# Kernel optimization log

Measured on AMD Instinct MI355X. Metric: run time of the kernel, lower is better.

Reference implementation:

```python
import jax, jax.numpy as jnp
import numpy as np

HEAD_SIZE = 64
EMBED_DIM = 1024

def setup_inputs() -> dict:
    key = jax.random.key(0)
    kx, kq, kk, kv = jax.random.split(key, 4)
    B, T, C, H = 8, 2048, EMBED_DIM, HEAD_SIZE
    scale = 1.0 / np.sqrt(C)
    x = jax.random.normal(kx, (B, T, C), dtype=jnp.float32)
    # nn.Linear(C, H, bias=False): weight (H, C); store as (C, H) for x @ W
    Wq = jax.random.normal(kq, (C, H), dtype=jnp.float32) * scale
    Wk = jax.random.normal(kk, (C, H), dtype=jnp.float32) * scale
    Wv = jax.random.normal(kv, (C, H), dtype=jnp.float32) * scale
    return {"x": x, "Wq": Wq, "Wk": Wk, "Wv": Wv}

def reference(x, Wq, Wk, Wv):
    B, T, C = x.shape
    H = Wq.shape[1]
    q = x @ Wq  # (B, T, H)
    k = x @ Wk
    v = x @ Wv
    # scaled scores with causal mask (tril)
    wei = jnp.einsum('bth,bsh->bts', q, k) * (H ** -0.5)  # (B, T, T)
    causal = jnp.tril(jnp.ones((T, T), dtype=bool))
    wei = jnp.where(causal, wei, -jnp.inf)
    wei = jax.nn.softmax(wei, axis=-1)
    out = jnp.einsum('bts,bsh->bth', wei, v)  # (B, T, H)
    return out
```

## Files before the change

### kernel.cpp

```cpp
#include <hip/hip_runtime.h>

#define T_SEQ 2048
#define C_DIM 1024
#define H_DIM 64
#define B_DIM 8
#define NROW (B_DIM * T_SEQ)

typedef __attribute__((ext_vector_type(8))) short short8;
typedef __attribute__((ext_vector_type(4))) float f32x4;

__device__ __forceinline__ short f2bf(float f) {
  unsigned u = __builtin_bit_cast(unsigned, f);
  u += 0x7fffu + ((u >> 16) & 1u);
  return (short)(u >> 16);
}

__global__ __launch_bounds__(256) void w_prep(
    const float* __restrict__ Wq, const float* __restrict__ Wk,
    const float* __restrict__ Wv, short* __restrict__ Wt2) {
  const int unit = blockIdx.x * 256 + threadIdx.x;
  const int lane = unit & 63;
  const int t = unit >> 6;
  const int kh = t & 3;
  const int g = t >> 2;
  const int ntg = g % 12;
  const int kc = g / 12;
  const int n16 = lane & 15, quad = lane >> 4;
  const int mat = ntg >> 2;
  const int h = (ntg & 3) * 16 + n16;
  const int kb = kc * 128 + kh * 32 + quad * 8;
  const float* W = (mat == 0) ? Wq : (mat == 1 ? Wk : Wv);
  short8 v;
#pragma unroll
  for (int e = 0; e < 8; ++e) v[e] = f2bf(W[(size_t)(kb + e) * H_DIM + h]);
  *(short8*)(Wt2 + (size_t)unit * 8) = v;
}

__device__ __forceinline__ int lds_addr(int tile, int kh, int qd, int nn) {
  return tile * 2048 + kh * 512 + (qd * 16 + (nn ^ ((kh * 4 + qd) & 7))) * 8;
}

__global__ __launch_bounds__(256, 2) void qkv_gemm(
    const float* __restrict__ x, const short* __restrict__ Wt2,
    short* __restrict__ q, short* __restrict__ k, short* __restrict__ vt) {
  __shared__ __align__(16) short As[2][4096];
  const int tid = threadIdx.x;
  const int w = tid >> 6, lane = tid & 63;
  const int n16 = lane & 15, quad = lane >> 4;
  const int row0 = blockIdx.x * 32;

  f32x4 acc[2][3];
#pragma unroll
  for (int mt = 0; mt < 2; ++mt)
#pragma unroll
    for (int ln = 0; ln < 3; ++ln) acc[mt][ln] = (f32x4){0.f, 0.f, 0.f, 0.f};

  const int u20 = tid, u21 = 256 + tid;
  const int sr0 = u20 >> 4, f0 = u20 & 15;
  const int sr1 = u21 >> 4, f1 = u21 & 15;
  const float* ap0 = x + (size_t)(row0 + sr0) * C_DIM + f0 * 8;
  const float* ap1 = x + (size_t)(row0 + sr1) * C_DIM + f1 * 8;
  const int soff0 = lds_addr(sr0 >> 4, f0 >> 2, f0 & 3, sr0 & 15);
  const int soff1 = lds_addr(sr1 >> 4, f1 >> 2, f1 & 3, sr1 & 15);

  int swz[4];
#pragma unroll
  for (int kh = 0; kh < 4; ++kh)
    swz[kh] = (quad * 16 + (n16 ^ ((kh * 4 + quad) & 7))) * 8;

  const short* bbase = Wt2 + (size_t)(w * 3) * 2048 + (size_t)lane * 8;

  float4 astg[2][4];
  short8 bfr[12];

#define STAGE_A(d, p)                                      \
  {                                                        \
    short8 av0, av1;                                       \
    _Pragma("unroll") for (int e = 0; e < 4; ++e) {        \
      av0[e] = f2bf(((const float*)&astg[d][0])[e]);       \
      av0[e + 4] = f2bf(((const float*)&astg[d][1])[e]);   \
      av1[e] = f2bf(((const float*)&astg[d][2])[e]);       \
      av1[e + 4] = f2bf(((const float*)&astg[d][3])[e]);   \
    }                                                      \
    *(short8*)(&As[p][0] + soff0) = av0;                   \
    *(short8*)(&As[p][0] + soff1) = av1;                   \
  }

  astg[0][0] = *(const float4*)(ap0);
  astg[0][1] = *(const float4*)(ap0 + 4);
  astg[0][2] = *(const float4*)(ap1);
  astg[0][3] = *(const float4*)(ap1 + 4);
  astg[1][0] = *(const float4*)(ap0 + 128);
  astg[1][1] = *(const float4*)(ap0 + 132);
  astg[1][2] = *(const float4*)(ap1 + 128);
  astg[1][3] = *(const float4*)(ap1 + 132);
#pragma unroll
  for (int ln = 0; ln < 3; ++ln)
#pragma unroll
    for (int kh = 0; kh < 4; ++kh)
      bfr[ln * 4 + kh] = *(const short8*)(bbase + ln * 2048 + kh * 512);
  STAGE_A(0, 0);
  asm volatile("s_waitcnt lgkmcnt(0)" ::: "memory");
  __builtin_amdgcn_sched_barrier(0);
  __builtin_amdgcn_s_barrier();
  __builtin_amdgcn_sched_barrier(0);

#pragma unroll
  for (int kc = 0; kc < 8; ++kc) {
    const short* asb = &As[kc & 1][0];
#pragma unroll
    for (int kh = 0; kh < 4; ++kh) {
      const short8 a0 = *(const short8*)(asb + kh * 512 + swz[kh]);
      const short8 a1 = *(const short8*)(asb + 2048 + kh * 512 + swz[kh]);
#pragma unroll
      for (int ln = 0; ln < 3; ++ln) {
        acc[0][ln] = __builtin_amdgcn_mfma_f32_16x16x32_bf16(
            a0, bfr[ln * 4 + kh], acc[0][ln], 0, 0, 0);
        acc[1][ln] = __builtin_amdgcn_mfma_f32_16x16x32_bf16(
            a1, bfr[ln * 4 + kh], acc[1][ln], 0, 0, 0);
      }
    }
    if (kc < 7) {
      const short* bc = bbase + (size_t)(kc + 1) * 24576;
#pragma unroll
      for (int ln = 0; ln < 3; ++ln)
#pragma unroll
        for (int kh = 0; kh < 4; ++kh)
          bfr[ln * 4 + kh] = *(const short8*)(bc + ln * 2048 + kh * 512);
      if (kc < 6) {
        astg[kc & 1][0] = *(const float4*)(ap0 + (kc + 2) * 128);
        astg[kc & 1][1] = *(const float4*)(ap0 + (kc + 2) * 128 + 4);
        astg[kc & 1][2] = *(const float4*)(ap1 + (kc + 2) * 128);
        astg[kc & 1][3] = *(const float4*)(ap1 + (kc + 2) * 128 + 4);
      }
      STAGE_A((kc + 1) & 1, (kc + 1) & 1);
      asm volatile("s_waitcnt lgkmcnt(0)" ::: "memory");
      __builtin_amdgcn_sched_barrier(0);
      __builtin_amdgcn_s_barrier();
      __builtin_amdgcn_sched_barrier(0);
    }
  }
#undef STAGE_A

  const int b = row0 >> 11;
#pragma unroll
  for (int mt = 0; mt < 2; ++mt)
#pragma unroll
    for (int ln = 0; ln < 3; ++ln) {
      const int ntg = w * 3 + ln;
      const int mat = ntg >> 2;
      const int cl = (ntg & 3) * 16 + n16;
#pragma unroll
      for (int r = 0; r < 4; ++r) {
        const int row = row0 + mt * 16 + quad * 4 + r;
        const float v = acc[mt][ln][r];
        if (mat == 0)
          q[(size_t)row * H_DIM + cl] = f2bf(v * 0.125f);
        else if (mat == 1)
          k[(size_t)row * H_DIM + cl] = f2bf(v);
        else
          vt[((size_t)b * H_DIM + cl) * T_SEQ + (row & (T_SEQ - 1))] = f2bf(v);
      }
    }
}

__global__ __launch_bounds__(256) void attn_mfma(
    const short* __restrict__ q, const short* __restrict__ k,
    const short* __restrict__ vt, float* __restrict__ out) {
  __shared__ __align__(16) short pbuf[4][1024];
  __shared__ __align__(16) float oshare[3][1024];
  __shared__ __align__(16) float lshare[3][256];
  const int tid = threadIdx.x;
  const int w = tid >> 6;
  const int lane = tid & 63;
  const int n16 = lane & 15, quad = lane >> 4;
  const int b = blockIdx.x & 7;
  const int qt = (T_SEQ / 16 - 1) - (blockIdx.x >> 3);
  const int r0 = qt * 16;

  const short* qb = q + ((size_t)b * T_SEQ + r0) * H_DIM;
  const short* kb = k + (size_t)b * T_SEQ * H_DIM;
  const short* vb = vt + (size_t)b * H_DIM * T_SEQ;

  const short8 aq0 = *(const short8*)(qb + (size_t)n16 * H_DIM + quad * 8);
  const short8 aq1 = *(const short8*)(qb + (size_t)n16 * H_DIM + 32 + quad * 8);

  f32x4 O[4];
#pragma unroll
  for (int i = 0; i < 4; ++i) O[i] = (f32x4){0.f, 0.f, 0.f, 0.f};
  float lsum[4] = {0.f, 0.f, 0.f, 0.f};

  const int nj = (r0 + 16 + 63) >> 6;
  for (int jt = w; jt < nj; jt += 4) {
    const int j0 = jt * 64;

    short8 bk[4][2];
#pragma unroll
    for (int nt = 0; nt < 4; ++nt) {
      const short* kp = kb + (size_t)(j0 + nt * 16 + n16) * H_DIM + quad * 8;
      bk[nt][0] = *(const short8*)kp;
      bk[nt][1] = *(const short8*)(kp + 32);
    }

    f32x4 s[4];
#pragma unroll
    for (int nt = 0; nt < 4; ++nt) {
      f32x4 z = (f32x4){0.f, 0.f, 0.f, 0.f};
      z = __builtin_amdgcn_mfma_f32_16x16x32_bf16(aq0, bk[nt][0], z, 0, 0, 0);
      z = __builtin_amdgcn_mfma_f32_16x16x32_bf16(aq1, bk[nt][1], z, 0, 0, 0);
      s[nt] = z;
    }

    const bool full = (j0 + 64 <= r0);
#pragma unroll
    for (int nt = 0; nt < 4; ++nt) {
      const int base =
          (nt >> 1) * 512 + ((((nt & 1) << 1) | (n16 >> 3)) * 128) + (n16 & 7);
#pragma unroll
      for (int r = 0; r < 4; ++r) {
        float p;
        if (full) {
          p = __expf(s[nt][r]);
        } else {
          const int j = j0 + nt * 16 + n16;
          const int row = r0 + quad * 4 + r;
          p = (j <= row) ? __expf(s[nt][r]) : 0.f;
        }
        lsum[r] += p;
        pbuf[w][base + (quad * 4 + r) * 8] = f2bf(p);
      }
    }

    short8 bv[4][2];
#pragma unroll
    for (int ht = 0; ht < 4; ++ht)
#pragma unroll
      for (int kh = 0; kh < 2; ++kh)
        bv[ht][kh] = *(const short8*)(vb + (size_t)(ht * 16 + n16) * T_SEQ +
                                      j0 + kh * 32 + quad * 8);

    const short8 ap0 = *(const short8*)(&pbuf[w][0] + lane * 8);
    const short8 ap1 = *(const short8*)(&pbuf[w][0] + 512 + lane * 8);

#pragma unroll
    for (int ht = 0; ht < 4; ++ht) {
      O[ht] = __builtin_amdgcn_mfma_f32_16x16x32_bf16(ap0, bv[ht][0], O[ht], 0, 0, 0);
      O[ht] = __builtin_amdgcn_mfma_f32_16x16x32_bf16(ap1, bv[ht][1], O[ht], 0, 0, 0);
    }
  }

  if (w != 0) {
#pragma unroll
    for (int ht = 0; ht < 4; ++ht)
#pragma unroll
      for (int r = 0; r < 4; ++r)
        oshare[w - 1][(ht * 4 + r) * 64 + lane] = O[ht][r];
#pragma unroll
    for (int r = 0; r < 4; ++r) lshare[w - 1][r * 64 + lane] = lsum[r];
  }
  __syncthreads();
  if (w == 0) {
#pragma unroll
    for (int ht = 0; ht < 4; ++ht)
#pragma unroll
      for (int r = 0; r < 4; ++r) {
        float a = O[ht][r];
#pragma unroll
        for (int ow = 0; ow < 3; ++ow) a += oshare[ow][(ht * 4 + r) * 64 + lane];
        O[ht][r] = a;
      }
#pragma unroll
    for (int r = 0; r < 4; ++r) {
      float vsum = lsum[r];
#pragma unroll
      for (int ow = 0; ow < 3; ++ow) vsum += lshare[ow][r * 64 + lane];
      vsum += __shfl_xor(vsum, 1);
      vsum += __shfl_xor(vsum, 2);
      vsum += __shfl_xor(vsum, 4);
      vsum += __shfl_xor(vsum, 8);
      lsum[r] = vsum;
    }
#pragma unroll
    for (int ht = 0; ht < 4; ++ht)
#pragma unroll
      for (int r = 0; r < 4; ++r)
        out[((size_t)b * T_SEQ + r0 + quad * 4 + r) * H_DIM + ht * 16 + n16] =
            O[ht][r] / lsum[r];
  }
}

extern "C" void kernel_launch(void* const* d_in, const int* in_sizes, int n_in,
                              void* d_out, int out_size, void* d_ws,
                              size_t ws_size, hipStream_t stream) {
  const float* x = (const float*)d_in[0];
  const float* Wq = (const float*)d_in[1];
  const float* Wk = (const float*)d_in[2];
  const float* Wv = (const float*)d_in[3];

  char* ws = (char*)d_ws;
  short* Wt = (short*)ws;
  short* q = (short*)(ws + 3 * 64 * 1024 * 2);
  short* kk = (short*)(ws + 3 * 64 * 1024 * 2 + 2097152);
  short* vt = (short*)(ws + 3 * 64 * 1024 * 2 + 2 * 2097152);

  w_prep<<<96, 256, 0, stream>>>(Wq, Wk, Wv, Wt);
  qkv_gemm<<<NROW / 32, 256, 0, stream>>>(x, Wt, q, kk, vt);
  attn_mfma<<<B_DIM * (T_SEQ / 16), 256, 0, stream>>>(q, kk, vt, (float*)d_out);
}
```

Measured before the change: 143.2 us.

## Pair short and long causal query tiles per block to share K/V loads

Each attention block now handles two 16-row query tiles, one near the start and one near the end of the sequence (pa and 127-pa). This balances causal work across blocks and reuses each loaded K and V tile for both query tiles where they overlap. It halves the grid and doubles LDS use and per-thread accumulators, which raises register pressure and may lower occupancy.

```diff
diff --git a/kernel.cpp b/kernel.cpp
--- a/kernel.cpp
+++ b/kernel.cpp
@@ -167,32 +167,44 @@
 __global__ __launch_bounds__(256) void attn_mfma(
     const short* __restrict__ q, const short* __restrict__ k,
     const short* __restrict__ vt, float* __restrict__ out) {
-  __shared__ __align__(16) short pbuf[4][1024];
-  __shared__ __align__(16) float oshare[3][1024];
-  __shared__ __align__(16) float lshare[3][256];
+  __shared__ __align__(16) short pbuf[4][2048];
+  __shared__ __align__(16) float oshare[3][2048];
+  __shared__ __align__(16) float lshare[3][512];
   const int tid = threadIdx.x;
   const int w = tid >> 6;
   const int lane = tid & 63;
   const int n16 = lane & 15, quad = lane >> 4;
   const int b = blockIdx.x & 7;
-  const int qt = (T_SEQ / 16 - 1) - (blockIdx.x >> 3);
-  const int r0 = qt * 16;
-
-  const short* qb = q + ((size_t)b * T_SEQ + r0) * H_DIM;
+  const int pa = blockIdx.x >> 3;
+  const int r0a = pa * 16;
+  const int r0b = (127 - pa) * 16;
+
   const short* kb = k + (size_t)b * T_SEQ * H_DIM;
   const short* vb = vt + (size_t)b * H_DIM * T_SEQ;
-
-  const short8 aq0 = *(const short8*)(qb + (size_t)n16 * H_DIM + quad * 8);
-  const short8 aq1 = *(const short8*)(qb + (size_t)n16 * H_DIM + 32 + quad * 8);
-
-  f32x4 O[4];
-#pragma unroll
-  for (int i = 0; i < 4; ++i) O[i] = (f32x4){0.f, 0.f, 0.f, 0.f};
-  float lsum[4] = {0.f, 0.f, 0.f, 0.f};
-
-  const int nj = (r0 + 16 + 63) >> 6;
+  const short* qpa = q + ((size_t)b * T_SEQ + r0a) * H_DIM;
+  const short* qpb = q + ((size_t)b * T_SEQ + r0b) * H_DIM;
+
+  short8 aqA[2], aqB[2];
+  aqA[0] = *(const short8*)(qpa + (size_t)n16 * H_DIM + quad * 8);
+  aqA[1] = *(const short8*)(qpa + (size_t)n16 * H_DIM + 32 + quad * 8);
+  aqB[0] = *(const short8*)(qpb + (size_t)n16 * H_DIM + quad * 8);
+  aqB[1] = *(const short8*)(qpb + (size_t)n16 * H_DIM + 32 + quad * 8);
+
+  f32x4 OA[4], OB[4];
+#pragma unroll
+  for (int i = 0; i < 4; ++i) {
+    OA[i] = (f32x4){0.f, 0.f, 0.f, 0.f};
+    OB[i] = (f32x4){0.f, 0.f, 0.f, 0.f};
+  }
+  float lsA[4] = {0.f, 0.f, 0.f, 0.f};
+  float lsB[4] = {0.f, 0.f, 0.f, 0.f};
+
+  const int nj = (r0b + 16 + 63) >> 6;
+  const int njA = (r0a + 16 + 63) >> 6;
+
   for (int jt = w; jt < nj; jt += 4) {
     const int j0 = jt * 64;
+    const bool actA = (jt < njA);
 
     short8 bk[4][2];
 #pragma unroll
@@ -202,16 +214,26 @@
       bk[nt][1] = *(const short8*)(kp + 32);
     }
 
-    f32x4 s[4];
+    f32x4 sB[4];
 #pragma unroll
     for (int nt = 0; nt < 4; ++nt) {
       f32x4 z = (f32x4){0.f, 0.f, 0.f, 0.f};
-      z = __builtin_amdgcn_mfma_f32_16x16x32_bf16(aq0, bk[nt][0], z, 0, 0, 0);
-      z = __builtin_amdgcn_mfma_f32_16x16x32_bf16(aq1, bk[nt][1], z, 0, 0, 0);
-      s[nt] = z;
-    }
-
-    const bool full = (j0 + 64 <= r0);
+      z = __builtin_amdgcn_mfma_f32_16x16x32_bf16(aqB[0], bk[nt][0], z, 0, 0, 0);
+      z = __builtin_amdgcn_mfma_f32_16x16x32_bf16(aqB[1], bk[nt][1], z, 0, 0, 0);
+      sB[nt] = z;
+    }
+    f32x4 sA[4];
+    if (actA) {
+#pragma unroll
+      for (int nt = 0; nt < 4; ++nt) {
+        f32x4 z = (f32x4){0.f, 0.f, 0.f, 0.f};
+        z = __builtin_amdgcn_mfma_f32_16x16x32_bf16(aqA[0], bk[nt][0], z, 0, 0, 0);
+        z = __builtin_amdgcn_mfma_f32_16x16x32_bf16(aqA[1], bk[nt][1], z, 0, 0, 0);
+        sA[nt] = z;
+      }
+    }
+
+    const bool fullB = (j0 + 64 <= r0b);
 #pragma unroll
     for (int nt = 0; nt < 4; ++nt) {
       const int base =
@@ -219,15 +241,36 @@
 #pragma unroll
       for (int r = 0; r < 4; ++r) {
         float p;
-        if (full) {
-          p = __expf(s[nt][r]);
+        if (fullB) {
+          p = __expf(sB[nt][r]);
         } else {
           const int j = j0 + nt * 16 + n16;
-          const int row = r0 + quad * 4 + r;
-          p = (j <= row) ? __expf(s[nt][r]) : 0.f;
+          const int row = r0b + quad * 4 + r;
+          p = (j <= row) ? __expf(sB[nt][r]) : 0.f;
         }
-        lsum[r] += p;
-        pbuf[w][base + (quad * 4 + r) * 8] = f2bf(p);
+        lsB[r] += p;
+        pbuf[w][1024 + base + (quad * 4 + r) * 8] = f2bf(p);
+      }
+    }
+    if (actA) {
+      const bool fullA = (j0 + 64 <= r0a);
+#pragma unroll
+      for (int nt = 0; nt < 4; ++nt) {
+        const int base =
+            (nt >> 1) * 512 + ((((nt & 1) << 1) | (n16 >> 3)) * 128) + (n16 & 7);
+#pragma unroll
+        for (int r = 0; r < 4; ++r) {
+          float p;
+          if (fullA) {
+            p = __expf(sA[nt][r]);
+          } else {
+            const int j = j0 + nt * 16 + n16;
+            const int row = r0a + quad * 4 + r;
+            p = (j <= row) ? __expf(sA[nt][r]) : 0.f;
+          }
+          lsA[r] += p;
+          pbuf[w][base + (quad * 4 + r) * 8] = f2bf(p);
+        }
       }
     }
 
@@ -239,13 +282,21 @@
         bv[ht][kh] = *(const short8*)(vb + (size_t)(ht * 16 + n16) * T_SEQ +
                                       j0 + kh * 32 + quad * 8);
 
-    const short8 ap0 = *(const short8*)(&pbuf[w][0] + lane * 8);
-    const short8 ap1 = *(const short8*)(&pbuf[w][0] + 512 + lane * 8);
-
+    const short8 apB0 = *(const short8*)(&pbuf[w][1024] + lane * 8);
+    const short8 apB1 = *(const short8*)(&pbuf[w][1536] + lane * 8);
 #pragma unroll
     for (int ht = 0; ht < 4; ++ht) {
-      O[ht] = __builtin_amdgcn_mfma_f32_16x16x32_bf16(ap0, bv[ht][0], O[ht], 0, 0, 0);
-      O[ht] = __builtin_amdgcn_mfma_f32_16x16x32_bf16(ap1, bv[ht][1], O[ht], 0, 0, 0);
+      OB[ht] = __builtin_amdgcn_mfma_f32_16x16x32_bf16(apB0, bv[ht][0], OB[ht], 0, 0, 0);
+      OB[ht] = __builtin_amdgcn_mfma_f32_16x16x32_bf16(apB1, bv[ht][1], OB[ht], 0, 0, 0);
+    }
+    if (actA) {
+      const short8 apA0 = *(const short8*)(&pbuf[w][0] + lane * 8);
+      const short8 apA1 = *(const short8*)(&pbuf[w][512] + lane * 8);
+#pragma unroll
+      for (int ht = 0; ht < 4; ++ht) {
+        OA[ht] = __builtin_amdgcn_mfma_f32_16x16x32_bf16(apA0, bv[ht][0], OA[ht], 0, 0, 0);
+        OA[ht] = __builtin_amdgcn_mfma_f32_16x16x32_bf16(apA1, bv[ht][1], OA[ht], 0, 0, 0);
+      }
     }
   }
 
@@ -253,10 +304,15 @@
 #pragma unroll
     for (int ht = 0; ht < 4; ++ht)
 #pragma unroll
-      for (int r = 0; r < 4; ++r)
-        oshare[w - 1][(ht * 4 + r) * 64 + lane] = O[ht][r];
-#pragma unroll
-    for (int r = 0; r < 4; ++r) lshare[w - 1][r * 64 + lane] = lsum[r];
+      for (int r = 0; r < 4; ++r) {
+        oshare[w - 1][(ht * 4 + r) * 64 + lane] = OA[ht][r];
+        oshare[w - 1][1024 + (ht * 4 + r) * 64 + lane] = OB[ht][r];
+      }
+#pragma unroll
+    for (int r = 0; r < 4; ++r) {
+      lshare[w - 1][r * 64 + lane] = lsA[r];
+      lshare[w - 1][256 + r * 64 + lane] = lsB[r];
+    }
   }
   __syncthreads();
   if (w == 0) {
@@ -264,28 +320,43 @@
     for (int ht = 0; ht < 4; ++ht)
 #pragma unroll
       for (int r = 0; r < 4; ++r) {
-        float a = O[ht][r];
-#pragma unroll
-        for (int ow = 0; ow < 3; ++ow) a += oshare[ow][(ht * 4 + r) * 64 + lane];
-        O[ht][r] = a;
+        float a = OA[ht][r], bb = OB[ht][r];
+#pragma unroll
+        for (int ow = 0; ow < 3; ++ow) {
+          a += oshare[ow][(ht * 4 + r) * 64 + lane];
+          bb += oshare[ow][1024 + (ht * 4 + r) * 64 + lane];
+        }
+        OA[ht][r] = a;
+        OB[ht][r] = bb;
       }
 #pragma unroll
     for (int r = 0; r < 4; ++r) {
-      float vsum = lsum[r];
-#pragma unroll
-      for (int ow = 0; ow < 3; ++ow) vsum += lshare[ow][r * 64 + lane];
-      vsum += __shfl_xor(vsum, 1);
-      vsum += __shfl_xor(vsum, 2);
-      vsum += __shfl_xor(vsum, 4);
-      vsum += __shfl_xor(vsum, 8);
-      lsum[r] = vsum;
+      float va = lsA[r], vb2 = lsB[r];
+#pragma unroll
+      for (int ow = 0; ow < 3; ++ow) {
+        va += lshare[ow][r * 64 + lane];
+        vb2 += lshare[ow][256 + r * 64 + lane];
+      }
+      va += __shfl_xor(va, 1);
+      va += __shfl_xor(va, 2);
+      va += __shfl_xor(va, 4);
+      va += __shfl_xor(va, 8);
+      vb2 += __shfl_xor(vb2, 1);
+      vb2 += __shfl_xor(vb2, 2);
+      vb2 += __shfl_xor(vb2, 4);
+      vb2 += __shfl_xor(vb2, 8);
+      lsA[r] = va;
+      lsB[r] = vb2;
     }
 #pragma unroll
     for (int ht = 0; ht < 4; ++ht)
 #pragma unroll
-      for (int r = 0; r < 4; ++r)
-        out[((size_t)b * T_SEQ + r0 + quad * 4 + r) * H_DIM + ht * 16 + n16] =
-            O[ht][r] / lsum[r];
+      for (int r = 0; r < 4; ++r) {
+        out[((size_t)b * T_SEQ + r0a + quad * 4 + r) * H_DIM + ht * 16 + n16] =
+            OA[ht][r] / lsA[r];
+        out[((size_t)b * T_SEQ + r0b + quad * 4 + r) * H_DIM + ht * 16 + n16] =
+            OB[ht][r] / lsB[r];
+      }
   }
 }
 
@@ -305,5 +376,5 @@
 
   w_prep<<<96, 256, 0, stream>>>(Wq, Wk, Wv, Wt);
   qkv_gemm<<<NROW / 32, 256, 0, stream>>>(x, Wt, q, kk, vt);
-  attn_mfma<<<B_DIM * (T_SEQ / 16), 256, 0, stream>>>(q, kk, vt, (float*)d_out);
-}
+  attn_mfma<<<B_DIM * (T_SEQ / 32), 256, 0, stream>>>(q, kk, vt, (float*)d_out);
+}
```

Result: faster. 137.0 us (-4.3%).

## Process four balanced query tiles per block and exchange P via lane shuffles

Applied to the files above, without the earlier changes.

Each attention block now handles four 16-row query tiles, paired front and back so causal work is balanced, and reuses each loaded K/V tile across all four. The QK^T MFMA is transposed so the P fragments can be rearranged into A-operand layout with cross-lane shuffles and packed bf16 conversion, replacing the LDS round-trip. Block count drops by four, which cuts redundant K/V loads. In exchange it raises register pressure (16 accumulators per wave) and LDS for the final reduction.

```diff
diff --git a/kernel.cpp b/kernel.cpp
--- a/kernel.cpp
+++ b/kernel.cpp
@@ -8,11 +8,18 @@
 
 typedef __attribute__((ext_vector_type(8))) short short8;
 typedef __attribute__((ext_vector_type(4))) float f32x4;
+typedef __attribute__((ext_vector_type(4))) int i32x4;
 
 __device__ __forceinline__ short f2bf(float f) {
   unsigned u = __builtin_bit_cast(unsigned, f);
   u += 0x7fffu + ((u >> 16) & 1u);
   return (short)(u >> 16);
+}
+
+__device__ __forceinline__ unsigned pk_bf16(float lo, float hi) {
+  unsigned r;
+  asm("v_cvt_pk_bf16_f32 %0, %1, %2" : "=v"(r) : "v"(lo), "v"(hi));
+  return r;
 }
 
 __global__ __launch_bounds__(256) void w_prep(
@@ -167,31 +174,42 @@
 __global__ __launch_bounds__(256) void attn_mfma(
     const short* __restrict__ q, const short* __restrict__ k,
     const short* __restrict__ vt, float* __restrict__ out) {
-  __shared__ __align__(16) short pbuf[4][1024];
-  __shared__ __align__(16) float oshare[3][1024];
-  __shared__ __align__(16) float lshare[3][256];
+  __shared__ __align__(16) float oshare[3][4096];
+  __shared__ __align__(16) float lshare[3][1024];
   const int tid = threadIdx.x;
   const int w = tid >> 6;
   const int lane = tid & 63;
   const int n16 = lane & 15, quad = lane >> 4;
   const int b = blockIdx.x & 7;
-  const int qt = (T_SEQ / 16 - 1) - (blockIdx.x >> 3);
-  const int r0 = qt * 16;
-
-  const short* qb = q + ((size_t)b * T_SEQ + r0) * H_DIM;
+  const int g = blockIdx.x >> 3;
+
+  int r0t[4], nj[4];
+  r0t[0] = g * 16;
+  r0t[1] = (63 - g) * 16;
+  r0t[2] = (64 + g) * 16;
+  r0t[3] = (127 - g) * 16;
+#pragma unroll
+  for (int t = 0; t < 4; ++t) nj[t] = (r0t[t] + 79) >> 6;
+
   const short* kb = k + (size_t)b * T_SEQ * H_DIM;
   const short* vb = vt + (size_t)b * H_DIM * T_SEQ;
 
-  const short8 aq0 = *(const short8*)(qb + (size_t)n16 * H_DIM + quad * 8);
-  const short8 aq1 = *(const short8*)(qb + (size_t)n16 * H_DIM + 32 + quad * 8);
-
-  f32x4 O[4];
-#pragma unroll
-  for (int i = 0; i < 4; ++i) O[i] = (f32x4){0.f, 0.f, 0.f, 0.f};
-  float lsum[4] = {0.f, 0.f, 0.f, 0.f};
-
-  const int nj = (r0 + 16 + 63) >> 6;
-  for (int jt = w; jt < nj; jt += 4) {
+  short8 aq[4][2];
+#pragma unroll
+  for (int t = 0; t < 4; ++t) {
+    const short* qp = q + ((size_t)b * T_SEQ + r0t[t] + n16) * H_DIM;
+    aq[t][0] = *(const short8*)(qp + quad * 8);
+    aq[t][1] = *(const short8*)(qp + 32 + quad * 8);
+  }
+
+  f32x4 O[4][4];
+#pragma unroll
+  for (int t = 0; t < 4; ++t)
+#pragma unroll
+    for (int i = 0; i < 4; ++i) O[t][i] = (f32x4){0.f, 0.f, 0.f, 0.f};
+  float lssc[4] = {0.f, 0.f, 0.f, 0.f};
+
+  for (int jt = w; jt < nj[3]; jt += 4) {
     const int j0 = jt * 64;
 
     short8 bk[4][2];
@@ -202,32 +220,35 @@
       bk[nt][1] = *(const short8*)(kp + 32);
     }
 
-    f32x4 s[4];
-#pragma unroll
-    for (int nt = 0; nt < 4; ++nt) {
-      f32x4 z = (f32x4){0.f, 0.f, 0.f, 0.f};
-      z = __builtin_amdgcn_mfma_f32_16x16x32_bf16(aq0, bk[nt][0], z, 0, 0, 0);
-      z = __builtin_amdgcn_mfma_f32_16x16x32_bf16(aq1, bk[nt][1], z, 0, 0, 0);
-      s[nt] = z;
-    }
-
-    const bool full = (j0 + 64 <= r0);
-#pragma unroll
-    for (int nt = 0; nt < 4; ++nt) {
-      const int base =
-          (nt >> 1) * 512 + ((((nt & 1) << 1) | (n16 >> 3)) * 128) + (n16 & 7);
-#pragma unroll
-      for (int r = 0; r < 4; ++r) {
-        float p;
-        if (full) {
-          p = __expf(s[nt][r]);
-        } else {
-          const int j = j0 + nt * 16 + n16;
-          const int row = r0 + quad * 4 + r;
-          p = (j <= row) ? __expf(s[nt][r]) : 0.f;
+    unsigned wp[4][4][2];
+#pragma unroll
+    for (int t = 0; t < 4; ++t) {
+      if (jt < nj[t]) {
+        f32x4 s[4];
+#pragma unroll
+        for (int nt = 0; nt < 4; ++nt) {
+          f32x4 z = (f32x4){0.f, 0.f, 0.f, 0.f};
+          z = __builtin_amdgcn_mfma_f32_16x16x32_bf16(bk[nt][0], aq[t][0], z, 0, 0, 0);
+          z = __builtin_amdgcn_mfma_f32_16x16x32_bf16(bk[nt][1], aq[t][1], z, 0, 0, 0);
+          s[nt] = z;
         }
-        lsum[r] += p;
-        pbuf[w][base + (quad * 4 + r) * 8] = f2bf(p);
+        const bool full = (j0 + 64 <= r0t[t]);
+#pragma unroll
+        for (int nt = 0; nt < 4; ++nt) {
+          float p[4];
+#pragma unroll
+          for (int r = 0; r < 4; ++r) {
+            if (full) {
+              p[r] = __expf(s[nt][r]);
+            } else {
+              const int j = j0 + nt * 16 + quad * 4 + r;
+              p[r] = (j <= r0t[t] + n16) ? __expf(s[nt][r]) : 0.f;
+            }
+            lssc[t] += p[r];
+          }
+          wp[t][nt][0] = pk_bf16(p[0], p[1]);
+          wp[t][nt][1] = pk_bf16(p[2], p[3]);
+        }
       }
     }
 
@@ -239,53 +260,101 @@
         bv[ht][kh] = *(const short8*)(vb + (size_t)(ht * 16 + n16) * T_SEQ +
                                       j0 + kh * 32 + quad * 8);
 
-    const short8 ap0 = *(const short8*)(&pbuf[w][0] + lane * 8);
-    const short8 ap1 = *(const short8*)(&pbuf[w][0] + 512 + lane * 8);
-
-#pragma unroll
-    for (int ht = 0; ht < 4; ++ht) {
-      O[ht] = __builtin_amdgcn_mfma_f32_16x16x32_bf16(ap0, bv[ht][0], O[ht], 0, 0, 0);
-      O[ht] = __builtin_amdgcn_mfma_f32_16x16x32_bf16(ap1, bv[ht][1], O[ht], 0, 0, 0);
-    }
-  }
+#define EXCHANGE(WSRC, AP0, AP1)                                          \
+  {                                                                       \
+    i32x4 apw[2];                                                         \
+    _Pragma("unroll") for (int h = 0; h < 2; ++h) {                       \
+      _Pragma("unroll") for (int ww = 0; ww < 2; ++ww) {                  \
+        const unsigned wlo = WSRC[2 * h][ww];                             \
+        const unsigned whi = WSRC[2 * h + 1][ww];                         \
+        const unsigned pay16 = (quad >= 2) ? whi : wlo;                   \
+        const unsigned pay2 = (quad < 2) ? whi : wlo;                     \
+        const unsigned x16 = (unsigned)__shfl_xor((int)pay16, 16);        \
+        const unsigned x32 = (unsigned)__shfl_xor((int)pay2, 32);         \
+        const unsigned x48 = (unsigned)__shfl_xor((int)pay2, 48);        \
+        const unsigned lo =                                               \
+            quad == 0 ? wlo : quad == 1 ? x48 : quad == 2 ? x32 : x16;    \
+        const unsigned hi =                                               \
+            quad == 0 ? x16 : quad == 1 ? x32 : quad == 2 ? x48 : whi;    \
+        apw[h][ww] = (int)lo;                                             \
+        apw[h][2 + ww] = (int)hi;                                         \
+      }                                                                   \
+    }                                                                     \
+    AP0 = __builtin_bit_cast(short8, apw[0]);                             \
+    AP1 = __builtin_bit_cast(short8, apw[1]);                             \
+  }
+
+#pragma unroll
+    for (int t = 0; t < 4; ++t) {
+      if (jt < nj[t]) {
+        short8 ap0, ap1;
+        EXCHANGE(wp[t], ap0, ap1);
+#pragma unroll
+        for (int ht = 0; ht < 4; ++ht) {
+          O[t][ht] = __builtin_amdgcn_mfma_f32_16x16x32_bf16(ap0, bv[ht][0], O[t][ht], 0, 0, 0);
+          O[t][ht] = __builtin_amdgcn_mfma_f32_16x16x32_bf16(ap1, bv[ht][1], O[t][ht], 0, 0, 0);
+        }
+      }
+    }
+#undef EXCHANGE
+  }
+
+  float ls[4][4];
+#pragma unroll
+  for (int t = 0; t < 4; ++t)
+#pragma unroll
+    for (int r = 0; r < 4; ++r) {
+      const int src = (n16 & 3) * 16 + quad * 4 + r;
+      const float v = __shfl(lssc[t], src);
+      ls[t][r] = (n16 < 4) ? v : 0.f;
+    }
 
   if (w != 0) {
 #pragma unroll
-    for (int ht = 0; ht < 4; ++ht)
+    for (int t = 0; t < 4; ++t) {
+#pragma unroll
+      for (int ht = 0; ht < 4; ++ht)
+#pragma unroll
+        for (int r = 0; r < 4; ++r)
+          oshare[w - 1][t * 1024 + (ht * 4 + r) * 64 + lane] = O[t][ht][r];
 #pragma unroll
       for (int r = 0; r < 4; ++r)
-        oshare[w - 1][(ht * 4 + r) * 64 + lane] = O[ht][r];
-#pragma unroll
-    for (int r = 0; r < 4; ++r) lshare[w - 1][r * 64 + lane] = lsum[r];
+        lshare[w - 1][t * 256 + r * 64 + lane] = ls[t][r];
+    }
   }
   __syncthreads();
   if (w == 0) {
 #pragma unroll
-    for (int ht = 0; ht < 4; ++ht)
+    for (int t = 0; t < 4; ++t) {
+#pragma unroll
+      for (int ht = 0; ht < 4; ++ht)
+#pragma unroll
+        for (int r = 0; r < 4; ++r) {
+          float a = O[t][ht][r];
+#pragma unroll
+          for (int ow = 0; ow < 3; ++ow)
+            a += oshare[ow][t * 1024 + (ht * 4 + r) * 64 + lane];
+          O[t][ht][r] = a;
+        }
 #pragma unroll
       for (int r = 0; r < 4; ++r) {
-        float a = O[ht][r];
-#pragma unroll
-        for (int ow = 0; ow < 3; ++ow) a += oshare[ow][(ht * 4 + r) * 64 + lane];
-        O[ht][r] = a;
-      }
-#pragma unroll
-    for (int r = 0; r < 4; ++r) {
-      float vsum = lsum[r];
-#pragma unroll
-      for (int ow = 0; ow < 3; ++ow) vsum += lshare[ow][r * 64 + lane];
-      vsum += __shfl_xor(vsum, 1);
-      vsum += __shfl_xor(vsum, 2);
-      vsum += __shfl_xor(vsum, 4);
-      vsum += __shfl_xor(vsum, 8);
-      lsum[r] = vsum;
-    }
-#pragma unroll
-    for (int ht = 0; ht < 4; ++ht)
-#pragma unroll
-      for (int r = 0; r < 4; ++r)
-        out[((size_t)b * T_SEQ + r0 + quad * 4 + r) * H_DIM + ht * 16 + n16] =
-            O[ht][r] / lsum[r];
+        float va = ls[t][r];
+#pragma unroll
+        for (int ow = 0; ow < 3; ++ow)
+          va += lshare[ow][t * 256 + r * 64 + lane];
+        va += __shfl_xor(va, 1);
+        va += __shfl_xor(va, 2);
+        va += __shfl_xor(va, 4);
+        va += __shfl_xor(va, 8);
+        ls[t][r] = va;
+      }
+#pragma unroll
+      for (int ht = 0; ht < 4; ++ht)
+#pragma unroll
+        for (int r = 0; r < 4; ++r)
+          out[((size_t)b * T_SEQ + r0t[t] + quad * 4 + r) * H_DIM + ht * 16 +
+              n16] = O[t][ht][r] / ls[t][r];
+    }
   }
 }
 
@@ -305,5 +374,5 @@
 
   w_prep<<<96, 256, 0, stream>>>(Wq, Wk, Wv, Wt);
   qkv_gemm<<<NROW / 32, 256, 0, stream>>>(x, Wt, q, kk, vt);
-  attn_mfma<<<B_DIM * (T_SEQ / 16), 256, 0, stream>>>(q, kk, vt, (float*)d_out);
-}
+  attn_mfma<<<B_DIM * (T_SEQ / 64), 256, 0, stream>>>(q, kk, vt, (float*)d_out);
+}
```

Result: faster. 133.8 us (-6.5%).
